# Kernel tuning notes

Measured on AMD Instinct MI355X. Metric: run time of the kernel, lower is better.

Reference implementation:

```python
import jax, jax.numpy as jnp
import numpy as np

TOP_K = 8  # num_experts_per_tok


def setup_inputs() -> dict:
    key = jax.random.key(0)
    k1, k2, k3 = jax.random.split(key, 3)
    B, S, H, E = 4, 4096, 2048, 64
    hidden_states = jax.random.normal(k1, (B, S, H), dtype=jnp.float32)
    router_weight = jax.random.normal(k2, (E, H), dtype=jnp.float32)
    router_bias = jnp.zeros((E,), dtype=jnp.float32)
    expert_bias = jax.random.normal(k3, (E, H), dtype=jnp.float32) * 0.1
    return {
        "hidden_states": hidden_states,
        "router_weight": router_weight,
        "router_bias": router_bias,
        "expert_bias": expert_bias,
    }


def reference(hidden_states, router_weight, router_bias, expert_bias):
    B, S, H = hidden_states.shape
    flat = hidden_states.reshape(B * S, H)  # [T, H]
    # Router: linear -> softmax -> top-k
    logits = jnp.einsum("th,eh->te", flat, router_weight) + router_bias
    scores = jax.nn.softmax(logits, axis=-1)
    topk_w, topk_idx = jax.lax.top_k(scores, TOP_K)  # [T, K]
    # Dispatch/combine collapses to: combined[t,k] = x[t] + expert_bias[idx[t,k]]
    # output[t] = sum_k w[t,k] * combined[t,k]
    #          = x[t] * sum_k w[t,k] + sum_k w[t,k] * expert_bias[idx[t,k]]
    gathered_bias = expert_bias[topk_idx]  # [T, K, H]
    out = flat * jnp.sum(topk_w, axis=-1, keepdims=True) + jnp.einsum(
        "tk,tkh->th", topk_w, gathered_bias
    )
    return out.reshape(B, S, H)
```

## Files before the change

kernel.cpp:

```cpp
#include <hip/hip_runtime.h>
#include <hip/hip_bf16.h>
#include <float.h>

#define H 2048
#define E 64
#define TOPK 8
#define RTOK 16
#define TT 8
#define NT 512

typedef __attribute__((ext_vector_type(8))) short bf16x8;
typedef __attribute__((ext_vector_type(4))) float f32x4;
typedef __attribute__((ext_vector_type(4))) unsigned short us4;

__device__ __forceinline__ unsigned short f2bf(float f) {
  unsigned u = __float_as_uint(f);
  u += 0x7fffu + ((u >> 16) & 1u);
  return (unsigned short)(u >> 16);
}
__device__ __forceinline__ float bf2f(unsigned short s) {
  return __uint_as_float(((unsigned)s) << 16);
}
__device__ __forceinline__ float wred_max(float v) {
#pragma unroll
  for (int o = 32; o > 0; o >>= 1) v = fmaxf(v, __shfl_xor(v, o));
  return v;
}
__device__ __forceinline__ float wred_sum(float v) {
#pragma unroll
  for (int o = 32; o > 0; o >>= 1) v += __shfl_xor(v, o);
  return v;
}

__global__ __launch_bounds__(256) void cvt_kernel(const float* __restrict__ W,
                                                  const float* __restrict__ eb,
                                                  unsigned short* __restrict__ Wb,
                                                  unsigned short* __restrict__ Bb) {
  int i = (blockIdx.x * 256 + threadIdx.x) * 4;
  const float* src;
  unsigned short* dst;
  int off;
  if (i < E * H) { src = W; dst = Wb; off = i; }
  else           { src = eb; dst = Bb; off = i - E * H; }
  float4 v = *(const float4*)(src + off);
  us4 r;
  r[0] = f2bf(v.x); r[1] = f2bf(v.y); r[2] = f2bf(v.z); r[3] = f2bf(v.w);
  *(us4*)(dst + off) = r;
}

__global__ __launch_bounds__(512, 4) void router_kernel(
    const float* __restrict__ x, const unsigned short* __restrict__ Wb,
    const float* __restrict__ rb, float* __restrict__ msw_g,
    float* __restrict__ mw_g, int* __restrict__ mi_g) {
  __shared__ float lgs[8][RTOK][E + 1];
  const int tid = threadIdx.x;
  const int wv = tid >> 6, lane = tid & 63, quad = lane >> 4, m = lane & 15;
  const int t0 = blockIdx.x * RTOK;
  const int k0 = wv * (H / 8);

  f32x4 acc0 = {0.f,0.f,0.f,0.f}, acc1 = {0.f,0.f,0.f,0.f};
  f32x4 acc2 = {0.f,0.f,0.f,0.f}, acc3 = {0.f,0.f,0.f,0.f};
  const float* xp = x + (size_t)(t0 + m) * H + k0 + quad * 8;
  const unsigned short* wp = Wb + (size_t)m * H + k0 + quad * 8;
#pragma unroll
  for (int it = 0; it < H / 8 / 32; ++it) {
    float4 p = *(const float4*)(xp + it * 32);
    float4 q = *(const float4*)(xp + it * 32 + 4);
    bf16x8 av;
    av[0] = (short)f2bf(p.x); av[1] = (short)f2bf(p.y);
    av[2] = (short)f2bf(p.z); av[3] = (short)f2bf(p.w);
    av[4] = (short)f2bf(q.x); av[5] = (short)f2bf(q.y);
    av[6] = (short)f2bf(q.z); av[7] = (short)f2bf(q.w);
    bf16x8 b0 = *(const bf16x8*)(wp + (size_t)0 * 16 * H + it * 32);
    bf16x8 b1 = *(const bf16x8*)(wp + (size_t)1 * 16 * H + it * 32);
    bf16x8 b2 = *(const bf16x8*)(wp + (size_t)2 * 16 * H + it * 32);
    bf16x8 b3 = *(const bf16x8*)(wp + (size_t)3 * 16 * H + it * 32);
    acc0 = __builtin_amdgcn_mfma_f32_16x16x32_bf16(av, b0, acc0, 0, 0, 0);
    acc1 = __builtin_amdgcn_mfma_f32_16x16x32_bf16(av, b1, acc1, 0, 0, 0);
    acc2 = __builtin_amdgcn_mfma_f32_16x16x32_bf16(av, b2, acc2, 0, 0, 0);
    acc3 = __builtin_amdgcn_mfma_f32_16x16x32_bf16(av, b3, acc3, 0, 0, 0);
  }
#pragma unroll
  for (int r = 0; r < 4; ++r) {
    const int row = quad * 4 + r;
    lgs[wv][row][ 0 + m] = acc0[r];
    lgs[wv][row][16 + m] = acc1[r];
    lgs[wv][row][32 + m] = acc2[r];
    lgs[wv][row][48 + m] = acc3[r];
  }
  __syncthreads();

  const float rbl = rb[lane];
#pragma unroll
  for (int tt = 0; tt < 2; ++tt) {
    const int t = wv * 2 + tt;
    float l = rbl;
#pragma unroll
    for (int kq = 0; kq < 8; ++kq) l += lgs[kq][t][lane];
    const float mx = wred_max(l);
    const float p = expf(l - mx);
    const float inv = 1.f / wred_sum(p);
    float sumw = 0.f, lsel = l;
    float mywk = 0.f;
    int myoff = 0;
#pragma unroll
    for (int k = 0; k < TOPK; ++k) {
      const float mk = wred_max(lsel);
      const unsigned long long b = __ballot(lsel == mk);
      const int idx = __ffsll(b) - 1;
      const float wk = expf(mk - mx) * inv;
      sumw += wk;
      if (lane == k) { mywk = wk; myoff = idx * H; }
      if (lane == idx) lsel = -FLT_MAX;
    }
    const int tg = t0 + t;
    if (lane == 0) msw_g[tg] = sumw;
    if (lane < TOPK) {
      mw_g[(size_t)tg * TOPK + lane] = mywk;
      mi_g[(size_t)tg * TOPK + lane] = myoff;
    }
  }
}

__global__ __launch_bounds__(256, 4) void combine_kernel(
    const float* __restrict__ x, const unsigned short* __restrict__ Bb,
    const float* __restrict__ msw_g, const float* __restrict__ mw_g,
    const int* __restrict__ mi_g, float* __restrict__ out) {
  const int tid = threadIdx.x;
  const int wv = tid >> 6, lane = tid & 63;
  const int t = blockIdx.x * 4 + wv;
  const float sw = msw_g[t];
  const float4 w0 = *(const float4*)(mw_g + (size_t)t * TOPK);
  const float4 w1 = *(const float4*)(mw_g + (size_t)t * TOPK + 4);
  const int4  e0 = *(const int4*)(mi_g + (size_t)t * TOPK);
  const int4  e1 = *(const int4*)(mi_g + (size_t)t * TOPK + 4);
  const float wks[8] = {w0.x, w0.y, w0.z, w0.w, w1.x, w1.y, w1.z, w1.w};
  const int   ofs[8] = {e0.x, e0.y, e0.z, e0.w, e1.x, e1.y, e1.z, e1.w};
  const float* xr = x + (size_t)t * H;
  float* orow = out + (size_t)t * H;
#pragma unroll
  for (int ch = 0; ch < 4; ++ch) {
    const int c8 = ch * 512 + lane * 8;
    const float4 xa = *(const float4*)(xr + c8);
    const float4 xb = *(const float4*)(xr + c8 + 4);
    float o[8] = {xa.x * sw, xa.y * sw, xa.z * sw, xa.w * sw,
                  xb.x * sw, xb.y * sw, xb.z * sw, xb.w * sw};
#pragma unroll
    for (int k = 0; k < TOPK; ++k) {
      const bf16x8 bv = *(const bf16x8*)(Bb + ofs[k] + c8);
      const float wk = wks[k];
#pragma unroll
      for (int i = 0; i < 8; ++i) o[i] += wk * bf2f((unsigned short)bv[i]);
    }
    *(float4*)(orow + c8)     = make_float4(o[0], o[1], o[2], o[3]);
    *(float4*)(orow + c8 + 4) = make_float4(o[4], o[5], o[6], o[7]);
  }
}

template <bool USE_WS>
__global__ __launch_bounds__(NT, 8) void moe_kernel(
    const float* __restrict__ x, const float* __restrict__ W,
    const float* __restrict__ rb, const float* __restrict__ eb,
    const unsigned short* __restrict__ Wb, const unsigned short* __restrict__ Bb,
    float* __restrict__ out) {
  __shared__ unsigned short xl[TT][H + 8];
  __shared__ float lgp[2][TT][E + 1];
  __shared__ float msw[TT];
  __shared__ float mw[TT][TOPK];
  __shared__ int   mi[TT][TOPK];

  const int tid = threadIdx.x;
  const int t0  = blockIdx.x * TT;
  const int wv = tid >> 6, lane = tid & 63, quad = lane >> 4, m = lane & 15;

  {
    const float* row = x + (size_t)(t0 + wv) * H;
#pragma unroll
    for (int i = 0; i < 8; ++i) {
      const int c = (i * 64 + lane) * 4;
      float4 a = *(const float4*)(row + c);
      us4 ra;
      ra[0] = f2bf(a.x); ra[1] = f2bf(a.y); ra[2] = f2bf(a.z); ra[3] = f2bf(a.w);
      *(us4*)&xl[wv][c] = ra;
    }
  }
  __syncthreads();

  {
    const int eg = wv & 3, kh = wv >> 2;
    const int e = eg * 16 + m;
    const int k0 = kh * (H / 2);
    f32x4 acc = {0.f, 0.f, 0.f, 0.f};
    const unsigned short* xp = &xl[m & 7][k0 + quad * 8];
    if (USE_WS) {
      const unsigned short* wp = Wb + (size_t)e * H + k0 + quad * 8;
#pragma unroll 8
      for (int it = 0; it < H / 64; ++it) {
        bf16x8 av = *(const bf16x8*)(xp + it * 32);
        bf16x8 bv = *(const bf16x8*)(wp + it * 32);
        acc = __builtin_amdgcn_mfma_f32_16x16x32_bf16(av, bv, acc, 0, 0, 0);
      }
    } else {
      const float* wp = W + (size_t)e * H + k0 + quad * 8;
#pragma unroll 4
      for (int it = 0; it < H / 64; ++it) {
        bf16x8 av = *(const bf16x8*)(xp + it * 32);
        float4 p = *(const float4*)(wp + it * 32);
        float4 q = *(const float4*)(wp + it * 32 + 4);
        bf16x8 bv;
        bv[0] = (short)f2bf(p.x); bv[1] = (short)f2bf(p.y);
        bv[2] = (short)f2bf(p.z); bv[3] = (short)f2bf(p.w);
        bv[4] = (short)f2bf(q.x); bv[5] = (short)f2bf(q.y);
        bv[6] = (short)f2bf(q.z); bv[7] = (short)f2bf(q.w);
        acc = __builtin_amdgcn_mfma_f32_16x16x32_bf16(av, bv, acc, 0, 0, 0);
      }
    }
#pragma unroll
    for (int r = 0; r < 4; ++r) {
      const int row = quad * 4 + r;
      if (row < TT) lgp[kh][row][eg * 16 + m] = acc[r];
    }
  }
  __syncthreads();

  {
    const int t = wv;
    float l = lgp[0][t][lane] + lgp[1][t][lane] + rb[lane];
    const float mx = wred_max(l);
    const float p = expf(l - mx);
    const float inv = 1.f / wred_sum(p);
    float sumw = 0.f;
    float lsel = l;
#pragma unroll
    for (int k = 0; k < TOPK; ++k) {
      const float mk = wred_max(lsel);
      const unsigned long long b = __ballot(lsel == mk);
      const int idx = __ffsll(b) - 1;
      const float wk = expf(mk - mx) * inv;
      sumw += wk;
      if (lane == 0) { mw[t][k] = wk; mi[t][k] = idx * H; }
      if (lane == idx) lsel = -FLT_MAX;
    }
    if (lane == 0) msw[t] = sumw;
  }
  __syncthreads();

  {
    const int tg = tid >> 8;
    const int c8 = (tid & 255) * 8;
    const unsigned short* bbase = Bb + c8;
    const float* ebase = eb + c8;
#pragma unroll 1
    for (int tt = 0; tt < TT / 2; ++tt) {
      const int t = tg * (TT / 2) + tt;
      const float sw = msw[t];
      const float4 w0 = *(const float4*)&mw[t][0];
      const float4 w1 = *(const float4*)&mw[t][4];
      const int4  e0 = *(const int4*)&mi[t][0];
      const int4  e1 = *(const int4*)&mi[t][4];
      const float wks[8] = {w0.x, w0.y, w0.z, w0.w, w1.x, w1.y, w1.z, w1.w};
      const int   ofs[8] = {e0.x, e0.y, e0.z, e0.w, e1.x, e1.y, e1.z, e1.w};
      bf16x8 xv = *(const bf16x8*)&xl[t][c8];
      float o[8];
#pragma unroll
      for (int i = 0; i < 8; ++i) o[i] = bf2f((unsigned short)xv[i]) * sw;
#pragma unroll
      for (int k = 0; k < TOPK; ++k) {
        const float wk = wks[k];
        if (USE_WS) {
          bf16x8 bv = *(const bf16x8*)(bbase + ofs[k]);
#pragma unroll
          for (int i = 0; i < 8; ++i) o[i] += wk * bf2f((unsigned short)bv[i]);
        } else {
          const float* p = ebase + ofs[k];
          float4 p0 = *(const float4*)p;
          float4 p1 = *(const float4*)(p + 4);
          o[0] += wk * p0.x; o[1] += wk * p0.y; o[2] += wk * p0.z; o[3] += wk * p0.w;
          o[4] += wk * p1.x; o[5] += wk * p1.y; o[6] += wk * p1.z; o[7] += wk * p1.w;
        }
      }
      float* op = out + (size_t)(t0 + t) * H + c8;
      *(float4*)op       = make_float4(o[0], o[1], o[2], o[3]);
      *(float4*)(op + 4) = make_float4(o[4], o[5], o[6], o[7]);
    }
  }
}

extern "C" void kernel_launch(void* const* d_in, const int* in_sizes, int n_in,
                              void* d_out, int out_size, void* d_ws, size_t ws_size,
                              hipStream_t stream) {
  const float* x  = (const float*)d_in[0];
  const float* W  = (const float*)d_in[1];
  const float* rb = (const float*)d_in[2];
  const float* eb = (const float*)d_in[3];
  float* out = (float*)d_out;

  const int T = in_sizes[0] / H;
  const size_t szW = (size_t)E * H * sizeof(unsigned short);
  const size_t need_old = 2 * szW;
  const size_t meta_sz = (size_t)T * 4 + (size_t)T * TOPK * 4 * 2;
  const size_t need_new = 2 * szW + meta_sz;

  if (ws_size >= need_new) {
    unsigned short* Wb = (unsigned short*)d_ws;
    unsigned short* Bb = Wb + (size_t)E * H;
    float* msw_g = (float*)(Bb + (size_t)E * H);
    float* mw_g  = msw_g + T;
    int*   mi_g  = (int*)(mw_g + (size_t)T * TOPK);
    cvt_kernel<<<(2 * E * H) / (256 * 4), 256, 0, stream>>>(W, eb, Wb, Bb);
    router_kernel<<<T / RTOK, 512, 0, stream>>>(x, Wb, rb, msw_g, mw_g, mi_g);
    combine_kernel<<<T / 4, 256, 0, stream>>>(x, Bb, msw_g, mw_g, mi_g, out);
  } else if (ws_size >= need_old) {
    unsigned short* Wb = (unsigned short*)d_ws;
    unsigned short* Bb = Wb + (size_t)E * H;
    cvt_kernel<<<(2 * E * H) / (256 * 4), 256, 0, stream>>>(W, eb, Wb, Bb);
    moe_kernel<true><<<T / TT, NT, 0, stream>>>(x, W, rb, eb, Wb, Bb, out);
  } else {
    moe_kernel<false><<<T / TT, NT, 0, stream>>>(x, W, rb, eb, nullptr, nullptr, out);
  }
}
```

Measured before the change: 280.9 us.

## Fuse router and combine kernels, reusing bf16 x held in registers

```diff
diff --git a/kernel.cpp b/kernel.cpp
--- a/kernel.cpp
+++ b/kernel.cpp
@@ -5,7 +5,6 @@
 #define H 2048
 #define E 64
 #define TOPK 8
-#define RTOK 16
 #define TT 8
 #define NT 512
 
@@ -48,22 +47,27 @@
   *(us4*)(dst + off) = r;
 }
 
-__global__ __launch_bounds__(512, 4) void router_kernel(
+__global__ __launch_bounds__(512, 4) void moe_fused(
     const float* __restrict__ x, const unsigned short* __restrict__ Wb,
-    const float* __restrict__ rb, float* __restrict__ msw_g,
-    float* __restrict__ mw_g, int* __restrict__ mi_g) {
-  __shared__ float lgs[8][RTOK][E + 1];
+    const float* __restrict__ rb, const unsigned short* __restrict__ Bb,
+    float* __restrict__ out) {
+  __shared__ float lgs[8][16][E + 1];
+  __shared__ float msw[16];
+  __shared__ float mwS[16][TOPK];
+  __shared__ int   miS[16][TOPK];
+
   const int tid = threadIdx.x;
   const int wv = tid >> 6, lane = tid & 63, quad = lane >> 4, m = lane & 15;
-  const int t0 = blockIdx.x * RTOK;
+  const int t0 = blockIdx.x * 16;
   const int k0 = wv * (H / 8);
 
+  bf16x8 xa[8];
   f32x4 acc0 = {0.f,0.f,0.f,0.f}, acc1 = {0.f,0.f,0.f,0.f};
   f32x4 acc2 = {0.f,0.f,0.f,0.f}, acc3 = {0.f,0.f,0.f,0.f};
   const float* xp = x + (size_t)(t0 + m) * H + k0 + quad * 8;
   const unsigned short* wp = Wb + (size_t)m * H + k0 + quad * 8;
 #pragma unroll
-  for (int it = 0; it < H / 8 / 32; ++it) {
+  for (int it = 0; it < 8; ++it) {
     float4 p = *(const float4*)(xp + it * 32);
     float4 q = *(const float4*)(xp + it * 32 + 4);
     bf16x8 av;
@@ -71,6 +75,7 @@
     av[2] = (short)f2bf(p.z); av[3] = (short)f2bf(p.w);
     av[4] = (short)f2bf(q.x); av[5] = (short)f2bf(q.y);
     av[6] = (short)f2bf(q.z); av[7] = (short)f2bf(q.w);
+    xa[it] = av;
     bf16x8 b0 = *(const bf16x8*)(wp + (size_t)0 * 16 * H + it * 32);
     bf16x8 b1 = *(const bf16x8*)(wp + (size_t)1 * 16 * H + it * 32);
     bf16x8 b2 = *(const bf16x8*)(wp + (size_t)2 * 16 * H + it * 32);
@@ -90,70 +95,63 @@
   }
   __syncthreads();
 
-  const float rbl = rb[lane];
-#pragma unroll
-  for (int tt = 0; tt < 2; ++tt) {
-    const int t = wv * 2 + tt;
-    float l = rbl;
-#pragma unroll
-    for (int kq = 0; kq < 8; ++kq) l += lgs[kq][t][lane];
-    const float mx = wred_max(l);
-    const float p = expf(l - mx);
-    const float inv = 1.f / wred_sum(p);
-    float sumw = 0.f, lsel = l;
-    float mywk = 0.f;
-    int myoff = 0;
-#pragma unroll
-    for (int k = 0; k < TOPK; ++k) {
-      const float mk = wred_max(lsel);
-      const unsigned long long b = __ballot(lsel == mk);
-      const int idx = __ffsll(b) - 1;
-      const float wk = expf(mk - mx) * inv;
-      sumw += wk;
-      if (lane == k) { mywk = wk; myoff = idx * H; }
-      if (lane == idx) lsel = -FLT_MAX;
-    }
-    const int tg = t0 + t;
-    if (lane == 0) msw_g[tg] = sumw;
-    if (lane < TOPK) {
-      mw_g[(size_t)tg * TOPK + lane] = mywk;
-      mi_g[(size_t)tg * TOPK + lane] = myoff;
-    }
-  }
-}
-
-__global__ __launch_bounds__(256, 4) void combine_kernel(
-    const float* __restrict__ x, const unsigned short* __restrict__ Bb,
-    const float* __restrict__ msw_g, const float* __restrict__ mw_g,
-    const int* __restrict__ mi_g, float* __restrict__ out) {
-  const int tid = threadIdx.x;
-  const int wv = tid >> 6, lane = tid & 63;
-  const int t = blockIdx.x * 4 + wv;
-  const float sw = msw_g[t];
-  const float4 w0 = *(const float4*)(mw_g + (size_t)t * TOPK);
-  const float4 w1 = *(const float4*)(mw_g + (size_t)t * TOPK + 4);
-  const int4  e0 = *(const int4*)(mi_g + (size_t)t * TOPK);
-  const int4  e1 = *(const int4*)(mi_g + (size_t)t * TOPK + 4);
-  const float wks[8] = {w0.x, w0.y, w0.z, w0.w, w1.x, w1.y, w1.z, w1.w};
-  const int   ofs[8] = {e0.x, e0.y, e0.z, e0.w, e1.x, e1.y, e1.z, e1.w};
-  const float* xr = x + (size_t)t * H;
-  float* orow = out + (size_t)t * H;
-#pragma unroll
-  for (int ch = 0; ch < 4; ++ch) {
-    const int c8 = ch * 512 + lane * 8;
-    const float4 xa = *(const float4*)(xr + c8);
-    const float4 xb = *(const float4*)(xr + c8 + 4);
-    float o[8] = {xa.x * sw, xa.y * sw, xa.z * sw, xa.w * sw,
-                  xb.x * sw, xb.y * sw, xb.z * sw, xb.w * sw};
-#pragma unroll
-    for (int k = 0; k < TOPK; ++k) {
-      const bf16x8 bv = *(const bf16x8*)(Bb + ofs[k] + c8);
-      const float wk = wks[k];
-#pragma unroll
-      for (int i = 0; i < 8; ++i) o[i] += wk * bf2f((unsigned short)bv[i]);
-    }
-    *(float4*)(orow + c8)     = make_float4(o[0], o[1], o[2], o[3]);
-    *(float4*)(orow + c8 + 4) = make_float4(o[4], o[5], o[6], o[7]);
+  {
+    const float rbl = rb[lane];
+#pragma unroll
+    for (int tt = 0; tt < 2; ++tt) {
+      const int t = wv * 2 + tt;
+      float l = rbl;
+#pragma unroll
+      for (int kq = 0; kq < 8; ++kq) l += lgs[kq][t][lane];
+      const float mx = wred_max(l);
+      const float p = expf(l - mx);
+      const float inv = 1.f / wred_sum(p);
+      float sumw = 0.f, lsel = l;
+      float mywk = 0.f;
+      int myoff = 0;
+#pragma unroll
+      for (int k = 0; k < TOPK; ++k) {
+        const float mk = wred_max(lsel);
+        const unsigned long long b = __ballot(lsel == mk);
+        const int idx = __ffsll(b) - 1;
+        const float wk = expf(mk - mx) * inv;
+        sumw += wk;
+        if (lane == k) { mywk = wk; myoff = idx * H; }
+        if (lane == idx) lsel = -FLT_MAX;
+      }
+      if (lane == 0) msw[t] = sumw;
+      if (lane < TOPK) {
+        mwS[t][lane] = mywk;
+        miS[t][lane] = myoff;
+      }
+    }
+  }
+  __syncthreads();
+
+  {
+    const float sw = msw[m];
+    float wks[TOPK];
+    int   ofs[TOPK];
+#pragma unroll
+    for (int k = 0; k < TOPK; ++k) { wks[k] = mwS[m][k]; ofs[k] = miS[m][k]; }
+    float* op = out + (size_t)(t0 + m) * H + k0 + quad * 8;
+    const unsigned short* bb = Bb + k0 + quad * 8;
+#pragma unroll
+    for (int it = 0; it < 8; ++it) {
+      const bf16x8 xv = xa[it];
+      float o[8];
+#pragma unroll
+      for (int i = 0; i < 8; ++i) o[i] = bf2f((unsigned short)xv[i]) * sw;
+#pragma unroll
+      for (int k = 0; k < TOPK; ++k) {
+        const bf16x8 bv = *(const bf16x8*)(bb + ofs[k] + it * 32);
+        const float wk = wks[k];
+#pragma unroll
+        for (int i = 0; i < 8; ++i) o[i] += wk * bf2f((unsigned short)bv[i]);
+      }
+      *(float4*)(op + it * 32)     = make_float4(o[0], o[1], o[2], o[3]);
+      *(float4*)(op + it * 32 + 4) = make_float4(o[4], o[5], o[6], o[7]);
+    }
   }
 }
 
@@ -297,24 +295,13 @@
 
   const int T = in_sizes[0] / H;
   const size_t szW = (size_t)E * H * sizeof(unsigned short);
-  const size_t need_old = 2 * szW;
-  const size_t meta_sz = (size_t)T * 4 + (size_t)T * TOPK * 4 * 2;
-  const size_t need_new = 2 * szW + meta_sz;
-
-  if (ws_size >= need_new) {
-    unsigned short* Wb = (unsigned short*)d_ws;
-    unsigned short* Bb = Wb + (size_t)E * H;
-    float* msw_g = (float*)(Bb + (size_t)E * H);
-    float* mw_g  = msw_g + T;
-    int*   mi_g  = (int*)(mw_g + (size_t)T * TOPK);
-    cvt_kernel<<<(2 * E * H) / (256 * 4), 256, 0, stream>>>(W, eb, Wb, Bb);
-    router_kernel<<<T / RTOK, 512, 0, stream>>>(x, Wb, rb, msw_g, mw_g, mi_g);
-    combine_kernel<<<T / 4, 256, 0, stream>>>(x, Bb, msw_g, mw_g, mi_g, out);
-  } else if (ws_size >= need_old) {
+  const size_t need = 2 * szW;
+
+  if (ws_size >= need) {
     unsigned short* Wb = (unsigned short*)d_ws;
     unsigned short* Bb = Wb + (size_t)E * H;
     cvt_kernel<<<(2 * E * H) / (256 * 4), 256, 0, stream>>>(W, eb, Wb, Bb);
-    moe_kernel<true><<<T / TT, NT, 0, stream>>>(x, W, rb, eb, Wb, Bb, out);
+    moe_fused<<<T / 16, 512, 0, stream>>>(x, Wb, rb, Bb, out);
   } else {
     moe_kernel<false><<<T / TT, NT, 0, stream>>>(x, W, rb, eb, nullptr, nullptr, out);
   }
```

After: 307.8 us. +9.6%, slower.

## Pipeline router x-tiles into LDS via async global_load_lds with swizzle

Applied to the files above, without the earlier changes.

```diff
diff --git a/kernel.cpp b/kernel.cpp
--- a/kernel.cpp
+++ b/kernel.cpp
@@ -5,7 +5,8 @@
 #define H 2048
 #define E 64
 #define TOPK 8
-#define RTOK 16
+#define RTT 32
+#define NCH 32
 #define TT 8
 #define NT 512
 
@@ -30,6 +31,12 @@
 #pragma unroll
   for (int o = 32; o > 0; o >>= 1) v += __shfl_xor(v, o);
   return v;
+}
+
+__device__ __forceinline__ void gll16(const float* g, const float* l) {
+  __builtin_amdgcn_global_load_lds(
+      (const __attribute__((address_space(1))) void*)g,
+      (__attribute__((address_space(3))) void*)l, 16, 0, 0);
 }
 
 __global__ __launch_bounds__(256) void cvt_kernel(const float* __restrict__ W,
@@ -52,51 +59,63 @@
     const float* __restrict__ x, const unsigned short* __restrict__ Wb,
     const float* __restrict__ rb, float* __restrict__ msw_g,
     float* __restrict__ mw_g, int* __restrict__ mi_g) {
-  __shared__ float lgs[8][RTOK][E + 1];
+  __shared__ float xch[4][RTT][64];
+  __shared__ float lgs[RTT][E + 1];
+
   const int tid = threadIdx.x;
   const int wv = tid >> 6, lane = tid & 63, quad = lane >> 4, m = lane & 15;
-  const int t0 = blockIdx.x * RTOK;
-  const int k0 = wv * (H / 8);
-
-  f32x4 acc0 = {0.f,0.f,0.f,0.f}, acc1 = {0.f,0.f,0.f,0.f};
-  f32x4 acc2 = {0.f,0.f,0.f,0.f}, acc3 = {0.f,0.f,0.f,0.f};
-  const float* xp = x + (size_t)(t0 + m) * H + k0 + quad * 8;
-  const unsigned short* wp = Wb + (size_t)m * H + k0 + quad * 8;
-#pragma unroll
-  for (int it = 0; it < H / 8 / 32; ++it) {
-    float4 p = *(const float4*)(xp + it * 32);
-    float4 q = *(const float4*)(xp + it * 32 + 4);
-    bf16x8 av;
-    av[0] = (short)f2bf(p.x); av[1] = (short)f2bf(p.y);
-    av[2] = (short)f2bf(p.z); av[3] = (short)f2bf(p.w);
-    av[4] = (short)f2bf(q.x); av[5] = (short)f2bf(q.y);
-    av[6] = (short)f2bf(q.z); av[7] = (short)f2bf(q.w);
-    bf16x8 b0 = *(const bf16x8*)(wp + (size_t)0 * 16 * H + it * 32);
-    bf16x8 b1 = *(const bf16x8*)(wp + (size_t)1 * 16 * H + it * 32);
-    bf16x8 b2 = *(const bf16x8*)(wp + (size_t)2 * 16 * H + it * 32);
-    bf16x8 b3 = *(const bf16x8*)(wp + (size_t)3 * 16 * H + it * 32);
-    acc0 = __builtin_amdgcn_mfma_f32_16x16x32_bf16(av, b0, acc0, 0, 0, 0);
-    acc1 = __builtin_amdgcn_mfma_f32_16x16x32_bf16(av, b1, acc1, 0, 0, 0);
-    acc2 = __builtin_amdgcn_mfma_f32_16x16x32_bf16(av, b2, acc2, 0, 0, 0);
-    acc3 = __builtin_amdgcn_mfma_f32_16x16x32_bf16(av, b3, acc3, 0, 0, 0);
-  }
-#pragma unroll
-  for (int r = 0; r < 4; ++r) {
-    const int row = quad * 4 + r;
-    lgs[wv][row][ 0 + m] = acc0[r];
-    lgs[wv][row][16 + m] = acc1[r];
-    lgs[wv][row][32 + m] = acc2[r];
-    lgs[wv][row][48 + m] = acc3[r];
-  }
+  const int t0 = blockIdx.x * RTT;
+  const int tg = wv & 1, eg = wv >> 1;
+
+  const int sr = 4 * wv + (lane >> 4);
+  const int sj = lane & 15;
+  const int scol = ((sj * 16) ^ ((sr & 7) << 4)) >> 2;
+  const float* sgp = x + (size_t)(t0 + sr) * H + scol;
+
+  f32x4 acc = {0.f, 0.f, 0.f, 0.f};
+  const unsigned short* wp = Wb + (size_t)(eg * 16 + m) * H + quad * 8;
+
+  gll16(sgp + 0 * 64, &xch[0][4 * wv][0]);
+  gll16(sgp + 1 * 64, &xch[1][4 * wv][0]);
+
+  const int rbase = tg * 16 + m;
+  const int swz = (rbase & 7) << 4;
+
+#pragma unroll 1
+  for (int c = 0; c < NCH; ++c) {
+    if (c + 2 < NCH) {
+      gll16(sgp + (c + 2) * 64, &xch[(c + 2) & 3][4 * wv][0]);
+      asm volatile("s_waitcnt vmcnt(2)" ::: "memory");
+    } else {
+      asm volatile("s_waitcnt vmcnt(0)" ::: "memory");
+    }
+    __builtin_amdgcn_s_barrier();
+    const char* cb = (const char*)&xch[c & 3][0][0] + rbase * 256;
+#pragma unroll
+    for (int ks = 0; ks < 2; ++ks) {
+      const int b = ks * 128 + quad * 32;
+      const float4 f0 = *(const float4*)(cb + ((b +  0) ^ swz));
+      const float4 f1 = *(const float4*)(cb + ((b + 16) ^ swz));
+      bf16x8 av;
+      av[0] = (short)f2bf(f0.x); av[1] = (short)f2bf(f0.y);
+      av[2] = (short)f2bf(f0.z); av[3] = (short)f2bf(f0.w);
+      av[4] = (short)f2bf(f1.x); av[5] = (short)f2bf(f1.y);
+      av[6] = (short)f2bf(f1.z); av[7] = (short)f2bf(f1.w);
+      const bf16x8 bv = *(const bf16x8*)(wp + c * 64 + ks * 32);
+      acc = __builtin_amdgcn_mfma_f32_16x16x32_bf16(av, bv, acc, 0, 0, 0);
+    }
+  }
+
+#pragma unroll
+  for (int r = 0; r < 4; ++r)
+    lgs[tg * 16 + quad * 4 + r][eg * 16 + m] = acc[r];
   __syncthreads();
 
   const float rbl = rb[lane];
 #pragma unroll
-  for (int tt = 0; tt < 2; ++tt) {
-    const int t = wv * 2 + tt;
-    float l = rbl;
-#pragma unroll
-    for (int kq = 0; kq < 8; ++kq) l += lgs[kq][t][lane];
+  for (int tt = 0; tt < 4; ++tt) {
+    const int t = wv * 4 + tt;
+    float l = lgs[t][lane] + rbl;
     const float mx = wred_max(l);
     const float p = expf(l - mx);
     const float inv = 1.f / wred_sum(p);
@@ -106,18 +125,18 @@
 #pragma unroll
     for (int k = 0; k < TOPK; ++k) {
       const float mk = wred_max(lsel);
-      const unsigned long long b = __ballot(lsel == mk);
-      const int idx = __ffsll(b) - 1;
+      const unsigned long long bmask = __ballot(lsel == mk);
+      const int idx = __ffsll(bmask) - 1;
       const float wk = expf(mk - mx) * inv;
       sumw += wk;
       if (lane == k) { mywk = wk; myoff = idx * H; }
       if (lane == idx) lsel = -FLT_MAX;
     }
-    const int tg = t0 + t;
-    if (lane == 0) msw_g[tg] = sumw;
+    const int tgl = t0 + t;
+    if (lane == 0) msw_g[tgl] = sumw;
     if (lane < TOPK) {
-      mw_g[(size_t)tg * TOPK + lane] = mywk;
-      mi_g[(size_t)tg * TOPK + lane] = myoff;
+      mw_g[(size_t)tgl * TOPK + lane] = mywk;
+      mi_g[(size_t)tgl * TOPK + lane] = myoff;
     }
   }
 }
@@ -157,11 +176,9 @@
   }
 }
 
-template <bool USE_WS>
 __global__ __launch_bounds__(NT, 8) void moe_kernel(
     const float* __restrict__ x, const float* __restrict__ W,
     const float* __restrict__ rb, const float* __restrict__ eb,
-    const unsigned short* __restrict__ Wb, const unsigned short* __restrict__ Bb,
     float* __restrict__ out) {
   __shared__ unsigned short xl[TT][H + 8];
   __shared__ float lgp[2][TT][E + 1];
@@ -192,28 +209,18 @@
     const int k0 = kh * (H / 2);
     f32x4 acc = {0.f, 0.f, 0.f, 0.f};
     const unsigned short* xp = &xl[m & 7][k0 + quad * 8];
-    if (USE_WS) {
-      const unsigned short* wp = Wb + (size_t)e * H + k0 + quad * 8;
-#pragma unroll 8
-      for (int it = 0; it < H / 64; ++it) {
-        bf16x8 av = *(const bf16x8*)(xp + it * 32);
-        bf16x8 bv = *(const bf16x8*)(wp + it * 32);
-        acc = __builtin_amdgcn_mfma_f32_16x16x32_bf16(av, bv, acc, 0, 0, 0);
-      }
-    } else {
-      const float* wp = W + (size_t)e * H + k0 + quad * 8;
+    const float* wpp = W + (size_t)e * H + k0 + quad * 8;
 #pragma unroll 4
-      for (int it = 0; it < H / 64; ++it) {
-        bf16x8 av = *(const bf16x8*)(xp + it * 32);
-        float4 p = *(const float4*)(wp + it * 32);
-        float4 q = *(const float4*)(wp + it * 32 + 4);
-        bf16x8 bv;
-        bv[0] = (short)f2bf(p.x); bv[1] = (short)f2bf(p.y);
-        bv[2] = (short)f2bf(p.z); bv[3] = (short)f2bf(p.w);
-        bv[4] = (short)f2bf(q.x); bv[5] = (short)f2bf(q.y);
-        bv[6] = (short)f2bf(q.z); bv[7] = (short)f2bf(q.w);
-        acc = __builtin_amdgcn_mfma_f32_16x16x32_bf16(av, bv, acc, 0, 0, 0);
-      }
+    for (int it = 0; it < H / 64; ++it) {
+      bf16x8 av = *(const bf16x8*)(xp + it * 32);
+      float4 p = *(const float4*)(wpp + it * 32);
+      float4 q = *(const float4*)(wpp + it * 32 + 4);
+      bf16x8 bv;
+      bv[0] = (short)f2bf(p.x); bv[1] = (short)f2bf(p.y);
+      bv[2] = (short)f2bf(p.z); bv[3] = (short)f2bf(p.w);
+      bv[4] = (short)f2bf(q.x); bv[5] = (short)f2bf(q.y);
+      bv[6] = (short)f2bf(q.z); bv[7] = (short)f2bf(q.w);
+      acc = __builtin_amdgcn_mfma_f32_16x16x32_bf16(av, bv, acc, 0, 0, 0);
     }
 #pragma unroll
     for (int r = 0; r < 4; ++r) {
@@ -248,7 +255,6 @@
   {
     const int tg = tid >> 8;
     const int c8 = (tid & 255) * 8;
-    const unsigned short* bbase = Bb + c8;
     const float* ebase = eb + c8;
 #pragma unroll 1
     for (int tt = 0; tt < TT / 2; ++tt) {
@@ -267,17 +273,11 @@
 #pragma unroll
       for (int k = 0; k < TOPK; ++k) {
         const float wk = wks[k];
-        if (USE_WS) {
-          bf16x8 bv = *(const bf16x8*)(bbase + ofs[k]);
-#pragma unroll
-          for (int i = 0; i < 8; ++i) o[i] += wk * bf2f((unsigned short)bv[i]);
-        } else {
-          const float* p = ebase + ofs[k];
-          float4 p0 = *(const float4*)p;
-          float4 p1 = *(const float4*)(p + 4);
-          o[0] += wk * p0.x; o[1] += wk * p0.y; o[2] += wk * p0.z; o[3] += wk * p0.w;
-          o[4] += wk * p1.x; o[5] += wk * p1.y; o[6] += wk * p1.z; o[7] += wk * p1.w;
-        }
+        const float* p = ebase + ofs[k];
+        float4 p0 = *(const float4*)p;
+        float4 p1 = *(const float4*)(p + 4);
+        o[0] += wk * p0.x; o[1] += wk * p0.y; o[2] += wk * p0.z; o[3] += wk * p0.w;
+        o[4] += wk * p1.x; o[5] += wk * p1.y; o[6] += wk * p1.z; o[7] += wk * p1.w;
       }
       float* op = out + (size_t)(t0 + t) * H + c8;
       *(float4*)op       = make_float4(o[0], o[1], o[2], o[3]);
@@ -297,25 +297,19 @@
 
   const int T = in_sizes[0] / H;
   const size_t szW = (size_t)E * H * sizeof(unsigned short);
-  const size_t need_old = 2 * szW;
   const size_t meta_sz = (size_t)T * 4 + (size_t)T * TOPK * 4 * 2;
-  const size_t need_new = 2 * szW + meta_sz;
-
-  if (ws_size >= need_new) {
+  const size_t need = 2 * szW + meta_sz;
+
+  if (ws_size >= need) {
     unsigned short* Wb = (unsigned short*)d_ws;
     unsigned short* Bb = Wb + (size_t)E * H;
     float* msw_g = (float*)(Bb + (size_t)E * H);
     float* mw_g  = msw_g + T;
     int*   mi_g  = (int*)(mw_g + (size_t)T * TOPK);
     cvt_kernel<<<(2 * E * H) / (256 * 4), 256, 0, stream>>>(W, eb, Wb, Bb);
-    router_kernel<<<T / RTOK, 512, 0, stream>>>(x, Wb, rb, msw_g, mw_g, mi_g);
+    router_kernel<<<T / RTT, 512, 0, stream>>>(x, Wb, rb, msw_g, mw_g, mi_g);
     combine_kernel<<<T / 4, 256, 0, stream>>>(x, Bb, msw_g, mw_g, mi_g, out);
-  } else if (ws_size >= need_old) {
-    unsigned short* Wb = (unsigned short*)d_ws;
-    unsigned short* Bb = Wb + (size_t)E * H;
-    cvt_kernel<<<(2 * E * H) / (256 * 4), 256, 0, stream>>>(W, eb, Wb, Bb);
-    moe_kernel<true><<<T / TT, NT, 0, stream>>>(x, W, rb, eb, Wb, Bb, out);
   } else {
-    moe_kernel<false><<<T / TT, NT, 0, stream>>>(x, W, rb, eb, nullptr, nullptr, out);
-  }
-}
+    moe_kernel<<<T / TT, NT, 0, stream>>>(x, W, rb, eb, out);
+  }
+}
```

After: 280.4 us. No clear change (-0.2%).
